# Optimization experiments

Hardware: AMD Instinct MI355X
Metric: run time of the kernel (lower is better)

Reference implementation:

```python
import jax, jax.numpy as jnp
import numpy as np
from jax import lax

B, N, C = 4, 3072, 512
SAMPLE_RATIO = 0.25
CLUSTER_NUM = int(np.ceil(N * SAMPLE_RATIO))  # 768, static (mask=None, no 'r')
K = 5  # self.k, since k <= cluster_num


def setup_inputs() -> dict:
    key = jax.random.key(0)
    k1, = jax.random.split(key, 1)
    x = jax.random.normal(k1, (B, N, C), dtype=jnp.float32)
    # idx_token starts as identity mapping per batch (standard TCFormer init)
    idx_token = jnp.tile(jnp.arange(N, dtype=jnp.int32)[None, :], (B, 1))
    agg_weight = jnp.ones((B, N, 1), dtype=jnp.float32)
    return {"x": x, "idx_token": idx_token, "agg_weight": agg_weight}


def _cluster_dpc_knn(x):
    # runs under no_grad in torch -> stop_gradient here
    xs = lax.stop_gradient(x).astype(jnp.float32)
    sq = jnp.sum(xs * xs, axis=-1)  # [B,N]
    d2 = sq[:, :, None] + sq[:, None, :] - 2.0 * jnp.einsum('bnc,bmc->bnm', xs, xs)
    dist = jnp.sqrt(jnp.maximum(d2, 0.0)) / jnp.sqrt(jnp.float32(C))  # cdist / C**0.5
    # k nearest (smallest) distances
    neg_nearest, _ = lax.top_k(-dist, K)
    dist_nearest = -neg_nearest  # [B,N,K]
    density = jnp.exp(-jnp.mean(dist_nearest ** 2, axis=-1))
    density = density + jax.random.uniform(jax.random.key(42), density.shape, dtype=density.dtype) * 1e-6
    mask = (density[:, None, :] > density[:, :, None]).astype(x.dtype)  # [B,N,N]
    dist_max = jnp.max(dist.reshape(B, -1), axis=-1)[:, None, None]
    dist_min = jnp.min(dist * mask + dist_max * (1.0 - mask), axis=-1)  # [B,N]
    score = dist_min * density
    _, index_down = lax.top_k(score, CLUSTER_NUM)  # [B,cluster]
    # gather rows of dist at cluster centers, assign each token to nearest center
    dmat = jnp.take_along_axis(dist, index_down[:, :, None], axis=1)  # [B,cluster,N]
    idx_cluster = jnp.argmin(dmat, axis=1).astype(jnp.int32)  # [B,N]
    # force centers to map to their own cluster id
    idx_cluster = idx_cluster.at[jnp.arange(B)[:, None], index_down].set(
        jnp.broadcast_to(jnp.arange(CLUSTER_NUM, dtype=jnp.int32)[None, :], (B, CLUSTER_NUM)))
    return idx_cluster


def reference(x, idx_token, agg_weight):
    idx_cluster = _cluster_dpc_knn(x)
    # merge_tokens
    token_weight = jnp.ones((B, N, 1), dtype=x.dtype)
    idx = idx_cluster + jnp.arange(B, dtype=jnp.int32)[:, None] * CLUSTER_NUM  # [B,N]
    idx_flat = idx.reshape(-1)
    all_weight = jax.ops.segment_sum(token_weight.reshape(-1), idx_flat,
                                     num_segments=B * CLUSTER_NUM) + 1e-6  # [B*cluster]
    norm_weight = token_weight / all_weight[idx_flat].reshape(B, N, 1)  # [B,N,1]
    x_merged = jax.ops.segment_sum((x * norm_weight).reshape(B * N, C), idx_flat,
                                   num_segments=B * CLUSTER_NUM).reshape(B, CLUSTER_NUM, C)
    idx_token_new = jnp.take_along_axis(idx_cluster, idx_token, axis=1)  # [B,N]
    weight_t = jnp.take_along_axis(norm_weight, idx_token[:, :, None], axis=1)  # [B,N,1]
    agg_weight_new = agg_weight * weight_t
    return x_merged, agg_weight_new, idx_token_new, idx_cluster
```

## Files before the change

### kernel.cpp

```cpp
#include <hip/hip_runtime.h>
#include <math.h>
#include <float.h>

constexpr int B  = 4;
constexpr int N  = 3072;
constexpr int C  = 512;
constexpr int CL = 768;

typedef unsigned short u16;
typedef __attribute__((ext_vector_type(8))) short s16x8;
typedef __attribute__((ext_vector_type(4))) float f32x4;

__device__ __forceinline__ unsigned rotl32(unsigned v, int d) { return (v << d) | (v >> (32 - d)); }

__device__ inline void threefry2x32(unsigned k0, unsigned k1, unsigned c0, unsigned c1,
                                    unsigned& o0, unsigned& o1) {
  unsigned ks0 = k0, ks1 = k1, ks2 = 0x1BD11BDAu ^ k0 ^ k1;
  unsigned x0 = c0 + ks0, x1 = c1 + ks1;
#define TF_RND(r) { x0 += x1; x1 = rotl32(x1, (r)); x1 ^= x0; }
  TF_RND(13) TF_RND(15) TF_RND(26) TF_RND(6)  x0 += ks1; x1 += ks2 + 1u;
  TF_RND(17) TF_RND(29) TF_RND(16) TF_RND(24) x0 += ks2; x1 += ks0 + 2u;
  TF_RND(13) TF_RND(15) TF_RND(26) TF_RND(6)  x0 += ks0; x1 += ks1 + 3u;
  TF_RND(17) TF_RND(29) TF_RND(16) TF_RND(24) x0 += ks1; x1 += ks2 + 4u;
  TF_RND(13) TF_RND(15) TF_RND(26) TF_RND(6)  x0 += ks2; x1 += ks0 + 5u;
#undef TF_RND
  o0 = x0; o1 = x1;
}

__device__ inline float jax_uniform_bn(int f) {
  constexpr int HALF = (B * N) / 2;
  unsigned o0, o1, bits;
  if (f < HALF) { threefry2x32(0u, 42u, (unsigned)f, (unsigned)(f + HALF), o0, o1); bits = o0; }
  else          { threefry2x32(0u, 42u, (unsigned)(f - HALF), (unsigned)f, o0, o1); bits = o1; }
  return __uint_as_float((bits >> 9) | 0x3f800000u) - 1.0f;
}

__device__ __forceinline__ u16 bf16rn(float f) {
  unsigned u = __float_as_uint(f);
  unsigned r = u + 0x7FFFu + ((u >> 16) & 1u);
  return (u16)(r >> 16);
}
__device__ __forceinline__ float bf16tof(u16 h) {
  return __uint_as_float(((unsigned)h) << 16);
}

__global__ __launch_bounds__(64) void k_prep(const float* __restrict__ x, float* __restrict__ sq,
                                             u16* __restrict__ xhi, u16* __restrict__ xlo,
                                             int* __restrict__ counts,
                                             unsigned long long* __restrict__ packed) {
  int row = blockIdx.x;
  int lane = threadIdx.x;
  const float* xr = x + (size_t)row * C;
  u16* hr = xhi + (size_t)row * C;
  u16* lr = xlo + (size_t)row * C;
  float s = 0.f;
  for (int c = lane * 4; c < C; c += 256) {
    float4 v = *(const float4*)(xr + c);
    s += v.x * v.x + v.y * v.y + v.z * v.z + v.w * v.w;
    u16 h0 = bf16rn(v.x), h1 = bf16rn(v.y), h2 = bf16rn(v.z), h3 = bf16rn(v.w);
    u16 l0 = bf16rn(v.x - bf16tof(h0));
    u16 l1 = bf16rn(v.y - bf16tof(h1));
    u16 l2 = bf16rn(v.z - bf16tof(h2));
    u16 l3 = bf16rn(v.w - bf16tof(h3));
    uint2 hp, lp;
    hp.x = (unsigned)h0 | ((unsigned)h1 << 16); hp.y = (unsigned)h2 | ((unsigned)h3 << 16);
    lp.x = (unsigned)l0 | ((unsigned)l1 << 16); lp.y = (unsigned)l2 | ((unsigned)l3 << 16);
    *(uint2*)(hr + c) = hp;
    *(uint2*)(lr + c) = lp;
  }
  for (int o = 32; o > 0; o >>= 1) s += __shfl_down(s, o, 64);
  if (lane == 0) {
    sq[row] = s;
    packed[row] = ~0ull;
    if (row < B * CL) counts[row] = 0;
  }
}

__device__ __forceinline__ void ins5b(float t[5], float v) {
  float c = v;
  float n;
  n = fminf(t[0], c); c = fmaxf(t[0], c); t[0] = n;
  n = fminf(t[1], c); c = fmaxf(t[1], c); t[1] = n;
  n = fminf(t[2], c); c = fmaxf(t[2], c); t[2] = n;
  n = fminf(t[3], c); c = fmaxf(t[3], c); t[3] = n;
  t[4] = fminf(t[4], c);
}

constexpr int NT3 = N / 128;
constexpr int NTILE3 = NT3 * (NT3 + 1) / 2;

__global__ __launch_bounds__(256, 3) void k_distm(const u16* __restrict__ xhi, const u16* __restrict__ xlo,
                                                  const float* __restrict__ sq,
                                                  float* __restrict__ distbuf,
                                                  float* __restrict__ part5, int b0) {
  constexpr int ASTR = 40;
  __shared__ __align__(16) char smem[40960];
  u16* sAh = (u16*)smem;
  u16* sAl = sAh + 128 * ASTR;
  u16* sBh = sAl + 128 * ASTR;
  u16* sBl = sBh + 128 * ASTR;

  int bl = blockIdx.y, b = b0 + bl;
  int idx = blockIdx.x;
  int ti = 0, rem = idx;
  while (rem >= NT3 - ti) { rem -= NT3 - ti; ++ti; }
  int tj = ti + rem;
  int i0 = ti * 128, j0 = tj * 128;
  bool do_mirror = (ti != tj);

  const float* sqb = sq + (size_t)b * N;
  float* dist = distbuf + (size_t)bl * N * N;

  int tid = threadIdx.x;
  int srow = tid >> 1, shalf = (tid & 1) * 16;
  const u16* gAh = xhi + ((size_t)b * N + i0 + srow) * C + shalf;
  const u16* gAl = xlo + ((size_t)b * N + i0 + srow) * C + shalf;
  const u16* gBh = xhi + ((size_t)b * N + j0 + srow) * C + shalf;
  const u16* gBl = xlo + ((size_t)b * N + j0 + srow) * C + shalf;
  int wofs = srow * ASTR + shalf;

  int lane = tid & 63, w = tid >> 6;
  int wr = (w >> 1) * 64, wc = (w & 1) * 64;
  int l15 = lane & 15, l4 = lane >> 4;

  f32x4 acc[4][4];
#pragma unroll
  for (int rt = 0; rt < 4; ++rt)
#pragma unroll
    for (int ct = 0; ct < 4; ++ct)
#pragma unroll
      for (int e = 0; e < 4; ++e) acc[rt][ct][e] = 0.f;

  uint4 p0 = *(const uint4*)gAh, p1 = *(const uint4*)(gAh + 8);
  uint4 p2 = *(const uint4*)gAl, p3 = *(const uint4*)(gAl + 8);
  uint4 p4 = *(const uint4*)gBh, p5 = *(const uint4*)(gBh + 8);
  uint4 p6 = *(const uint4*)gBl, p7 = *(const uint4*)(gBl + 8);

  for (int k0 = 0; k0 < C; k0 += 32) {
    *(uint4*)&sAh[wofs] = p0; *(uint4*)&sAh[wofs + 8] = p1;
    *(uint4*)&sAl[wofs] = p2; *(uint4*)&sAl[wofs + 8] = p3;
    *(uint4*)&sBh[wofs] = p4; *(uint4*)&sBh[wofs + 8] = p5;
    *(uint4*)&sBl[wofs] = p6; *(uint4*)&sBl[wofs + 8] = p7;
    __syncthreads();
    int kn = k0 + 32;
    if (kn < C) {
      p0 = *(const uint4*)(gAh + kn); p1 = *(const uint4*)(gAh + kn + 8);
      p2 = *(const uint4*)(gAl + kn); p3 = *(const uint4*)(gAl + kn + 8);
      p4 = *(const uint4*)(gBh + kn); p5 = *(const uint4*)(gBh + kn + 8);
      p6 = *(const uint4*)(gBl + kn); p7 = *(const uint4*)(gBl + kn + 8);
    }
    s16x8 ah[4], al[4];
#pragma unroll
    for (int rt = 0; rt < 4; ++rt) {
      int ro = (wr + rt * 16 + l15) * ASTR + l4 * 8;
      ah[rt] = *(const s16x8*)&sAh[ro];
      al[rt] = *(const s16x8*)&sAl[ro];
    }
#pragma unroll
    for (int ct = 0; ct < 4; ++ct) {
      int co = (wc + ct * 16 + l15) * ASTR + l4 * 8;
      s16x8 bh = *(const s16x8*)&sBh[co];
      s16x8 bl = *(const s16x8*)&sBl[co];
#pragma unroll
      for (int rt = 0; rt < 4; ++rt) {
        acc[rt][ct] = __builtin_amdgcn_mfma_f32_16x16x32_bf16(ah[rt], bh, acc[rt][ct], 0, 0, 0);
        acc[rt][ct] = __builtin_amdgcn_mfma_f32_16x16x32_bf16(ah[rt], bl, acc[rt][ct], 0, 0, 0);
        acc[rt][ct] = __builtin_amdgcn_mfma_f32_16x16x32_bf16(al[rt], bh, acc[rt][ct], 0, 0, 0);
      }
    }
    __syncthreads();
  }

  const float SQC = 22.627416997969522f;
  float sqi[4][4], sqj[4];
#pragma unroll
  for (int rt = 0; rt < 4; ++rt)
#pragma unroll
    for (int r = 0; r < 4; ++r) sqi[rt][r] = sqb[i0 + wr + rt * 16 + l4 * 4 + r];
#pragma unroll
  for (int ct = 0; ct < 4; ++ct) sqj[ct] = sqb[j0 + wc + ct * 16 + l15];

#pragma unroll
  for (int rt = 0; rt < 4; ++rt)
#pragma unroll
    for (int ct = 0; ct < 4; ++ct)
#pragma unroll
      for (int r = 0; r < 4; ++r) {
        float d2 = fmaxf(sqi[rt][r] + sqj[ct] - 2.0f * acc[rt][ct][r], 0.0f);
        acc[rt][ct][r] = sqrtf(d2) / SQC;
      }

  constexpr int TSTR = 76;
  float* sT = (float*)smem + w * (32 * TSTR);

  float t5A[5] = {FLT_MAX, FLT_MAX, FLT_MAX, FLT_MAX, FLT_MAX};
  float mxA = 0.f;

#pragma unroll
  for (int p = 0; p < 2; ++p) {
#pragma unroll
    for (int cth = 0; cth < 2; ++cth) {
      int ct = p * 2 + cth;
      int cl = cth * 16 + l15;
#pragma unroll
      for (int rt = 0; rt < 4; ++rt)
#pragma unroll
        for (int r = 0; r < 4; ++r)
          sT[cl * TSTR + rt * 16 + l4 * 4 + r] = acc[rt][ct][r];
    }
    {
      int g4 = lane & 7, rbase = lane >> 3;
#pragma unroll
      for (int it = 0; it < 8; ++it) {
        int rl = it * 8 + rbase;
        float4 v = make_float4(sT[(4 * g4 + 0) * TSTR + rl],
                               sT[(4 * g4 + 1) * TSTR + rl],
                               sT[(4 * g4 + 2) * TSTR + rl],
                               sT[(4 * g4 + 3) * TSTR + rl]);
        *(float4*)(dist + (size_t)(i0 + wr + rl) * N + j0 + wc + p * 32 + 4 * g4) = v;
      }
    }
    if (do_mirror) {
      int cg = lane >> 4, rq = lane & 15;
#pragma unroll
      for (int cc = 0; cc < 8; ++cc) {
        int c = cc * 4 + cg;
        float4 v = *(const float4*)&sT[c * TSTR + rq * 4];
        *(float4*)(dist + (size_t)(j0 + wc + p * 32 + c) * N + i0 + wr + rq * 4) = v;
      }
    }
    for (int c = 0; c < 32; ++c) {
      float v = sT[c * TSTR + lane];
      mxA = fmaxf(mxA, v);
      ins5b(t5A, v);
    }
    if (do_mirror) {
      int cl = lane & 31, half = lane >> 5;
      float t5B[5] = {FLT_MAX, FLT_MAX, FLT_MAX, FLT_MAX, FLT_MAX};
      float mxB = 0.f;
      for (int k = 0; k < 32; ++k) {
        float v = sT[cl * TSTR + half * 32 + k];
        mxB = fmaxf(mxB, v);
        ins5b(t5B, v);
      }
      mxB = fmaxf(mxB, __shfl_xor(mxB, 32, 64));
      float o0 = __shfl_xor(t5B[0], 32, 64);
      float o1 = __shfl_xor(t5B[1], 32, 64);
      float o2 = __shfl_xor(t5B[2], 32, 64);
      float o3 = __shfl_xor(t5B[3], 32, 64);
      float o4 = __shfl_xor(t5B[4], 32, 64);
      ins5b(t5B, o0); ins5b(t5B, o1); ins5b(t5B, o2); ins5b(t5B, o3); ins5b(t5B, o4);
      if (half == 0) {
        int rowB = j0 + wc + p * 32 + cl;
        int slotB = ti * 2 + (wr >> 6);
        float* dst = part5 + (((size_t)bl * 48 + slotB) * 6) * N + rowB;
        dst[0] = t5B[0]; dst[(size_t)N] = t5B[1]; dst[2 * (size_t)N] = t5B[2];
        dst[3 * (size_t)N] = t5B[3]; dst[4 * (size_t)N] = t5B[4]; dst[5 * (size_t)N] = mxB;
      }
    }
  }
  {
    int rowA = i0 + wr + lane;
    int slotA = tj * 2 + (wc >> 6);
    float* dst = part5 + (((size_t)bl * 48 + slotA) * 6) * N + rowA;
    dst[0] = t5A[0]; dst[(size_t)N] = t5A[1]; dst[2 * (size_t)N] = t5A[2];
    dst[3 * (size_t)N] = t5A[3]; dst[4 * (size_t)N] = t5A[4]; dst[5 * (size_t)N] = mxA;
  }
}

__global__ __launch_bounds__(256) void k_dens(const float* __restrict__ part5,
                                              float* __restrict__ density,
                                              float* __restrict__ rowmax, int b0) {
  int g = blockIdx.x * 256 + threadIdx.x;
  int bl = g / N, r = g % N;
  int b = b0 + bl;
  const float* base = part5 + (size_t)bl * 48 * 6 * N + r;
  float t5[5] = {FLT_MAX, FLT_MAX, FLT_MAX, FLT_MAX, FLT_MAX};
  float mx = 0.f;
  for (int s = 0; s < 48; ++s) {
    const float* sp = base + (size_t)s * 6 * N;
    ins5b(t5, sp[0]);
    ins5b(t5, sp[(size_t)N]);
    ins5b(t5, sp[2 * (size_t)N]);
    ins5b(t5, sp[3 * (size_t)N]);
    ins5b(t5, sp[4 * (size_t)N]);
    mx = fmaxf(mx, sp[5 * (size_t)N]);
  }
  float sum = t5[0] * t5[0] + t5[1] * t5[1] + t5[2] * t5[2] + t5[3] * t5[3] + t5[4] * t5[4];
  density[b * N + r] = expf(-(sum / 5.0f)) + jax_uniform_bn(b * N + r) * 1e-6f;
  rowmax[b * N + r] = mx;
}

__global__ __launch_bounds__(1024) void k_dmax(const float* __restrict__ rowmax,
                                               float* __restrict__ distmax) {
  __shared__ float red[16];
  int b = blockIdx.x;
  int tid = threadIdx.x;
  const float* rb = rowmax + (size_t)b * N;
  float mx = 0.f;
  for (int j = tid; j < N; j += 1024) mx = fmaxf(mx, rb[j]);
#pragma unroll
  for (int m = 1; m < 64; m <<= 1) mx = fmaxf(mx, __shfl_xor(mx, m, 64));
  if ((tid & 63) == 0) red[tid >> 6] = mx;
  __syncthreads();
  if (tid == 0) {
    float r = red[0];
#pragma unroll
    for (int q = 1; q < 16; ++q) r = fmaxf(r, red[q]);
    distmax[b] = r;
  }
}

__global__ __launch_bounds__(256) void k_maskmin(const float* __restrict__ distbuf,
                                                 const float* __restrict__ density,
                                                 const float* __restrict__ distmax,
                                                 float* __restrict__ score, int b0) {
  __shared__ float sd[N];
  int tid = threadIdx.x;
  int wv = tid >> 6, lane = tid & 63;
  int i = blockIdx.x * 4 + wv;
  int bl = blockIdx.y, b = b0 + bl;
  const float* db = density + (size_t)b * N;
  for (int j = tid * 4; j < N; j += 1024) *(float4*)(sd + j) = *(const float4*)(db + j);
  __syncthreads();
  float di = sd[i];
  float dmax = distmax[b];
  const float* row = distbuf + ((size_t)bl * N + i) * N;
  float mn = dmax;
#pragma unroll
  for (int it = 0; it < N / 256; ++it) {
    int j = it * 256 + lane * 4;
    float4 v = *(const float4*)(row + j);
    float4 d = *(const float4*)(sd + j);
    mn = fminf(mn, (d.x > di) ? v.x : dmax);
    mn = fminf(mn, (d.y > di) ? v.y : dmax);
    mn = fminf(mn, (d.z > di) ? v.z : dmax);
    mn = fminf(mn, (d.w > di) ? v.w : dmax);
  }
#pragma unroll
  for (int m = 1; m < 64; m <<= 1) mn = fminf(mn, __shfl_xor(mn, m, 64));
  if (lane == 0) score[b * N + i] = mn * di;
}

__global__ __launch_bounds__(256) void k_rank(const float* __restrict__ score,
                                              int* __restrict__ index_down,
                                              int* __restrict__ rank, int b0) {
  __shared__ float ssc[N];
  int tid = threadIdx.x;
  int wv = tid >> 6, lane = tid & 63;
  int i = blockIdx.x * 4 + wv;
  int b = b0 + blockIdx.y;
  const float* sb = score + (size_t)b * N;
  for (int j = tid * 4; j < N; j += 1024) *(float4*)(ssc + j) = *(const float4*)(sb + j);
  __syncthreads();
  float si = ssc[i];
  int cnt = 0;
#pragma unroll
  for (int it = 0; it < N / 256; ++it) {
    int j = it * 256 + lane * 4;
    float4 v = *(const float4*)(ssc + j);
    cnt += (v.x > si) || (v.x == si && (j + 0) < i);
    cnt += (v.y > si) || (v.y == si && (j + 1) < i);
    cnt += (v.z > si) || (v.z == si && (j + 2) < i);
    cnt += (v.w > si) || (v.w == si && (j + 3) < i);
  }
#pragma unroll
  for (int m = 1; m < 64; m <<= 1) cnt += __shfl_xor(cnt, m, 64);
  if (lane == 0) {
    rank[b * N + i] = (cnt < CL) ? cnt : -1;
    if (cnt < CL) index_down[b * CL + cnt] = i;
  }
}

__global__ __launch_bounds__(256) void k_assign_part(const float* __restrict__ distbuf,
                                                     const int* __restrict__ index_down,
                                                     unsigned long long* __restrict__ packed, int b0) {
  constexpr int RCH = CL / 8;
  __shared__ int sid[RCH];
  int bl = blockIdx.z, b = b0 + bl;
  int r0 = blockIdx.y * RCH;
  int tid = threadIdx.x;
  for (int r = tid; r < RCH; r += 256) sid[r] = index_down[b * CL + r0 + r];
  __syncthreads();
  int j = blockIdx.x * 256 + tid;
  const float* base = distbuf + (size_t)bl * N * N;
  float best = FLT_MAX; int bestr = 0;
#pragma unroll 8
  for (int r = 0; r < RCH; ++r) {
    float d = base[(size_t)sid[r] * N + j];
    if (d < best) { best = d; bestr = r0 + r; }
  }
  unsigned long long key = ((unsigned long long)__float_as_uint(best) << 32) | (unsigned)bestr;
  atomicMin(&packed[b * N + j], key);
}

__global__ void k_assign_fin2(const unsigned long long* __restrict__ packed,
                              const int* __restrict__ rank,
                              int* __restrict__ idx_cluster, int* __restrict__ counts) {
  int g = blockIdx.x * 256 + threadIdx.x;
  int b = g / N;
  int r = rank[g];
  int cl = (r >= 0) ? r : (int)(unsigned)(packed[g] & 0xffffffffull);
  idx_cluster[g] = cl;
  atomicAdd(&counts[b * CL + cl], 1);
}

__global__ __launch_bounds__(1024) void k_scan(const int* __restrict__ counts,
                                               int* __restrict__ offsets, int* __restrict__ cursor) {
  constexpr int T = B * CL;
  __shared__ int sm[T];
  int tid = threadIdx.x;
  for (int p = tid; p < T; p += 1024) sm[p] = counts[p];
  __syncthreads();
  for (int off = 1; off < T; off <<= 1) {
    int v[3]; int n = 0;
    for (int p = tid; p < T; p += 1024) { v[n++] = (p >= off) ? sm[p - off] : 0; }
    __syncthreads();
    n = 0;
    for (int p = tid; p < T; p += 1024) { sm[p] += v[n++]; }
    __syncthreads();
  }
  for (int p = tid; p < T; p += 1024) {
    int e = sm[p] - counts[p];
    offsets[p] = e; cursor[p] = e;
  }
}

__global__ void k_fill(const int* __restrict__ idx_cluster, int* __restrict__ cursor,
                       int* __restrict__ members) {
  int g = blockIdx.x * 256 + threadIdx.x;
  int b = g / N, i = g % N;
  int seg = b * CL + idx_cluster[g];
  int pos = atomicAdd(&cursor[seg], 1);
  members[pos] = i;
}

__global__ __launch_bounds__(128) void k_gather(const float* __restrict__ x, const int* __restrict__ members,
                                                const int* __restrict__ offsets, const int* __restrict__ counts,
                                                float* __restrict__ out0) {
  int seg = blockIdx.x;
  int b = seg / CL;
  int cnt = counts[seg], off = offsets[seg];
  float nw = 1.0f / ((float)cnt + 1e-6f);
  int c = threadIdx.x * 4;
  const float* xb = x + (size_t)b * N * C;
  float4 acc = make_float4(0.f, 0.f, 0.f, 0.f);
  for (int m = 0; m < cnt; ++m) {
    int tok = members[off + m];
    float4 v = *(const float4*)(xb + (size_t)tok * C + c);
    acc.x += v.x * nw; acc.y += v.y * nw; acc.z += v.z * nw; acc.w += v.w * nw;
  }
  *(float4*)(out0 + (size_t)seg * C + c) = acc;
}

__global__ void k_final(const float* __restrict__ agg_weight, const int* __restrict__ idx_token,
                        const int* __restrict__ idx_cluster, const int* __restrict__ counts,
                        float* __restrict__ out1, float* __restrict__ out2, float* __restrict__ out3) {
  int g = blockIdx.x * 256 + threadIdx.x;
  int b = g / N;
  int it = idx_token[g];
  int clt = idx_cluster[b * N + it];
  float nwt = 1.0f / ((float)counts[b * CL + clt] + 1e-6f);
  out1[g] = agg_weight[g] * nwt;
  out2[g] = (float)clt;
  out3[g] = (float)idx_cluster[g];
}

extern "C" void kernel_launch(void* const* d_in, const int* in_sizes, int n_in,
                              void* d_out, int out_size, void* d_ws, size_t ws_size,
                              hipStream_t stream) {
  const float* x          = (const float*)d_in[0];
  const int*   idx_token  = (const int*)d_in[1];
  const float* agg_weight = (const float*)d_in[2];

  float* out0 = (float*)d_out;
  float* out1 = out0 + (size_t)B * CL * C;
  float* out2 = out1 + (size_t)B * N;
  float* out3 = out2 + (size_t)B * N;

  char* w = (char*)d_ws;
  auto carve = [&](size_t bytes) { char* p = w; w += (bytes + 255) & ~(size_t)255; return p; };
  float*    sq         = (float*)carve((size_t)B * N * 4);
  float*    density    = (float*)carve((size_t)B * N * 4);
  float*    score      = (float*)carve((size_t)B * N * 4);
  float*    rowmax     = (float*)carve((size_t)B * N * 4);
  float*    distmax    = (float*)carve((size_t)B * 4);
  int*      index_down = (int*)carve((size_t)B * CL * 4);
  int*      rank       = (int*)carve((size_t)B * N * 4);
  int*      idx_clus   = (int*)carve((size_t)B * N * 4);
  int*      counts     = (int*)carve((size_t)B * CL * 4);
  int*      offsets    = (int*)carve((size_t)B * CL * 4);
  int*      cursor     = (int*)carve((size_t)B * CL * 4);
  int*      members    = (int*)carve((size_t)B * N * 4);
  unsigned long long* packed = (unsigned long long*)carve((size_t)B * N * 8);
  u16*      xhi        = (u16*)carve((size_t)B * N * C * 2);
  u16*      xlo        = (u16*)carve((size_t)B * N * C * 2);
  float*    part5      = (float*)carve((size_t)B * 48 * 6 * N * 4);
  size_t used = (size_t)(w - (char*)d_ws);
  size_t per  = (size_t)N * N * 4;
  int nb_max = (ws_size > used) ? (int)((ws_size - used) / per) : 0;
  if (nb_max < 1) nb_max = 1;
  if (nb_max > B) nb_max = B;
  float* distbuf = (float*)w;

  k_prep<<<B * N, 64, 0, stream>>>(x, sq, xhi, xlo, counts, packed);

  for (int b0 = 0; b0 < B; b0 += nb_max) {
    int nb = (B - b0 < nb_max) ? (B - b0) : nb_max;
    k_distm<<<dim3(NTILE3, nb), 256, 0, stream>>>(xhi, xlo, sq, distbuf, part5, b0);
    k_dens<<<(nb * N) / 256, 256, 0, stream>>>(part5, density, rowmax, b0);
    k_dmax<<<nb, 1024, 0, stream>>>(rowmax + (size_t)b0 * N, distmax + b0);
    k_maskmin<<<dim3(N / 4, nb), 256, 0, stream>>>(distbuf, density, distmax, score, b0);
    k_rank<<<dim3(N / 4, nb), 256, 0, stream>>>(score, index_down, rank, b0);
    k_assign_part<<<dim3(N / 256, 8, nb), 256, 0, stream>>>(distbuf, index_down, packed, b0);
  }

  k_assign_fin2<<<(B * N) / 256, 256, 0, stream>>>(packed, rank, idx_clus, counts);
  k_scan<<<1, 1024, 0, stream>>>(counts, offsets, cursor);
  k_fill<<<(B * N) / 256, 256, 0, stream>>>(idx_clus, cursor, members);
  k_gather<<<B * CL, 128, 0, stream>>>(x, members, offsets, counts, out0);
  k_final<<<(B * N) / 256, 256, 0, stream>>>(agg_weight, idx_token, idx_clus, counts, out1, out2, out3);
}
```

Baseline: 301.7 us.

## Fuse post-distance stages into one cooperative persistent kernel with grid syncs

Replaces the chain of tail kernels (density, dmax, masked min, rank, assign, scan, fill, gather, final) with a single cooperative kernel of 256 blocks that separates the stages with grid.sync(). It also drops the batch chunking loop, so the distance matrix for all batches is computed in one launch. The aim is to remove per-kernel launch and drain gaps between the many small stages. The cost is that each stage now runs on a fixed 256-block grid, which can reduce parallelism in heavy stages such as the masked min (each wave now handles 12 rows) and the assign step (only 384 work units). It also assumes the workspace is large enough to hold all B distance matrices.

```diff
diff --git a/kernel.cpp b/kernel.cpp
--- a/kernel.cpp
+++ b/kernel.cpp
@@ -1,6 +1,9 @@
 #include <hip/hip_runtime.h>
+#include <hip/hip_cooperative_groups.h>
 #include <math.h>
 #include <float.h>
+
+namespace cg = cooperative_groups;
 
 constexpr int B  = 4;
 constexpr int N  = 3072;
@@ -268,202 +271,214 @@
   }
 }
 
-__global__ __launch_bounds__(256) void k_dens(const float* __restrict__ part5,
-                                              float* __restrict__ density,
-                                              float* __restrict__ rowmax, int b0) {
-  int g = blockIdx.x * 256 + threadIdx.x;
-  int bl = g / N, r = g % N;
-  int b = b0 + bl;
-  const float* base = part5 + (size_t)bl * 48 * 6 * N + r;
-  float t5[5] = {FLT_MAX, FLT_MAX, FLT_MAX, FLT_MAX, FLT_MAX};
-  float mx = 0.f;
-  for (int s = 0; s < 48; ++s) {
-    const float* sp = base + (size_t)s * 6 * N;
-    ins5b(t5, sp[0]);
-    ins5b(t5, sp[(size_t)N]);
-    ins5b(t5, sp[2 * (size_t)N]);
-    ins5b(t5, sp[3 * (size_t)N]);
-    ins5b(t5, sp[4 * (size_t)N]);
-    mx = fmaxf(mx, sp[5 * (size_t)N]);
-  }
-  float sum = t5[0] * t5[0] + t5[1] * t5[1] + t5[2] * t5[2] + t5[3] * t5[3] + t5[4] * t5[4];
-  density[b * N + r] = expf(-(sum / 5.0f)) + jax_uniform_bn(b * N + r) * 1e-6f;
-  rowmax[b * N + r] = mx;
-}
-
-__global__ __launch_bounds__(1024) void k_dmax(const float* __restrict__ rowmax,
-                                               float* __restrict__ distmax) {
-  __shared__ float red[16];
-  int b = blockIdx.x;
-  int tid = threadIdx.x;
-  const float* rb = rowmax + (size_t)b * N;
-  float mx = 0.f;
-  for (int j = tid; j < N; j += 1024) mx = fmaxf(mx, rb[j]);
-#pragma unroll
-  for (int m = 1; m < 64; m <<= 1) mx = fmaxf(mx, __shfl_xor(mx, m, 64));
-  if ((tid & 63) == 0) red[tid >> 6] = mx;
-  __syncthreads();
-  if (tid == 0) {
-    float r = red[0];
-#pragma unroll
-    for (int q = 1; q < 16; ++q) r = fmaxf(r, red[q]);
-    distmax[b] = r;
-  }
-}
-
-__global__ __launch_bounds__(256) void k_maskmin(const float* __restrict__ distbuf,
-                                                 const float* __restrict__ density,
-                                                 const float* __restrict__ distmax,
-                                                 float* __restrict__ score, int b0) {
-  __shared__ float sd[N];
+struct TailArgs {
+  const float* part5;
+  float* density;
+  float* rowmax;
+  float* distmax;
+  const float* distbuf;
+  float* score;
+  int* index_down;
+  int* rank;
+  unsigned long long* packed;
+  int* idx_cluster;
+  int* counts;
+  int* offsets;
+  int* cursor;
+  int* members;
+  const float* x;
+  const int* idx_token;
+  const float* agg_weight;
+  float* out0;
+  float* out1;
+  float* out2;
+  float* out3;
+};
+
+constexpr int TGRID = 256;
+
+__global__ __launch_bounds__(256) void k_tail(TailArgs a) {
+  cg::grid_group grid = cg::this_grid();
+  __shared__ float smf[N];
+  __shared__ float sred[16];
   int tid = threadIdx.x;
   int wv = tid >> 6, lane = tid & 63;
-  int i = blockIdx.x * 4 + wv;
-  int bl = blockIdx.y, b = b0 + bl;
-  const float* db = density + (size_t)b * N;
-  for (int j = tid * 4; j < N; j += 1024) *(float4*)(sd + j) = *(const float4*)(db + j);
-  __syncthreads();
-  float di = sd[i];
-  float dmax = distmax[b];
-  const float* row = distbuf + ((size_t)bl * N + i) * N;
-  float mn = dmax;
-#pragma unroll
-  for (int it = 0; it < N / 256; ++it) {
-    int j = it * 256 + lane * 4;
-    float4 v = *(const float4*)(row + j);
-    float4 d = *(const float4*)(sd + j);
-    mn = fminf(mn, (d.x > di) ? v.x : dmax);
-    mn = fminf(mn, (d.y > di) ? v.y : dmax);
-    mn = fminf(mn, (d.z > di) ? v.z : dmax);
-    mn = fminf(mn, (d.w > di) ? v.w : dmax);
-  }
-#pragma unroll
-  for (int m = 1; m < 64; m <<= 1) mn = fminf(mn, __shfl_xor(mn, m, 64));
-  if (lane == 0) score[b * N + i] = mn * di;
-}
-
-__global__ __launch_bounds__(256) void k_rank(const float* __restrict__ score,
-                                              int* __restrict__ index_down,
-                                              int* __restrict__ rank, int b0) {
-  __shared__ float ssc[N];
-  int tid = threadIdx.x;
-  int wv = tid >> 6, lane = tid & 63;
-  int i = blockIdx.x * 4 + wv;
-  int b = b0 + blockIdx.y;
-  const float* sb = score + (size_t)b * N;
-  for (int j = tid * 4; j < N; j += 1024) *(float4*)(ssc + j) = *(const float4*)(sb + j);
-  __syncthreads();
-  float si = ssc[i];
-  int cnt = 0;
-#pragma unroll
-  for (int it = 0; it < N / 256; ++it) {
-    int j = it * 256 + lane * 4;
-    float4 v = *(const float4*)(ssc + j);
-    cnt += (v.x > si) || (v.x == si && (j + 0) < i);
-    cnt += (v.y > si) || (v.y == si && (j + 1) < i);
-    cnt += (v.z > si) || (v.z == si && (j + 2) < i);
-    cnt += (v.w > si) || (v.w == si && (j + 3) < i);
-  }
-#pragma unroll
-  for (int m = 1; m < 64; m <<= 1) cnt += __shfl_xor(cnt, m, 64);
-  if (lane == 0) {
-    rank[b * N + i] = (cnt < CL) ? cnt : -1;
-    if (cnt < CL) index_down[b * CL + cnt] = i;
-  }
-}
-
-__global__ __launch_bounds__(256) void k_assign_part(const float* __restrict__ distbuf,
-                                                     const int* __restrict__ index_down,
-                                                     unsigned long long* __restrict__ packed, int b0) {
-  constexpr int RCH = CL / 8;
-  __shared__ int sid[RCH];
-  int bl = blockIdx.z, b = b0 + bl;
-  int r0 = blockIdx.y * RCH;
-  int tid = threadIdx.x;
-  for (int r = tid; r < RCH; r += 256) sid[r] = index_down[b * CL + r0 + r];
-  __syncthreads();
-  int j = blockIdx.x * 256 + tid;
-  const float* base = distbuf + (size_t)bl * N * N;
-  float best = FLT_MAX; int bestr = 0;
+  int gtid = blockIdx.x * 256 + tid;
+
+  for (int g = gtid; g < B * N; g += TGRID * 256) {
+    int b = g / N, r = g % N;
+    const float* base = a.part5 + (size_t)b * 48 * 6 * N + r;
+    float t5[5] = {FLT_MAX, FLT_MAX, FLT_MAX, FLT_MAX, FLT_MAX};
+    float mx = 0.f;
+    for (int s = 0; s < 48; ++s) {
+      const float* sp = base + (size_t)s * 6 * N;
+      ins5b(t5, sp[0]);
+      ins5b(t5, sp[(size_t)N]);
+      ins5b(t5, sp[2 * (size_t)N]);
+      ins5b(t5, sp[3 * (size_t)N]);
+      ins5b(t5, sp[4 * (size_t)N]);
+      mx = fmaxf(mx, sp[5 * (size_t)N]);
+    }
+    float sum = t5[0] * t5[0] + t5[1] * t5[1] + t5[2] * t5[2] + t5[3] * t5[3] + t5[4] * t5[4];
+    a.density[g] = expf(-(sum / 5.0f)) + jax_uniform_bn(g) * 1e-6f;
+    a.rowmax[g] = mx;
+  }
+  grid.sync();
+
+  if (blockIdx.x < B) {
+    int b = blockIdx.x;
+    float mx = 0.f;
+    for (int j = tid; j < N; j += 256) mx = fmaxf(mx, a.rowmax[b * N + j]);
+#pragma unroll
+    for (int m = 1; m < 64; m <<= 1) mx = fmaxf(mx, __shfl_xor(mx, m, 64));
+    if (lane == 0) sred[wv] = mx;
+    __syncthreads();
+    if (tid == 0)
+      a.distmax[b] = fmaxf(fmaxf(sred[0], sred[1]), fmaxf(sred[2], sred[3]));
+  }
+  grid.sync();
+
+  {
+    int b = blockIdx.x >> 6;
+    int blk = blockIdx.x & 63;
+    const float* db = a.density + (size_t)b * N;
+    for (int j = tid * 4; j < N; j += 1024) *(float4*)(smf + j) = *(const float4*)(db + j);
+    __syncthreads();
+    float dmax = a.distmax[b];
+    for (int t = 0; t < 12; ++t) {
+      int r = blk * 48 + wv * 12 + t;
+      float di = smf[r];
+      const float* row = a.distbuf + (size_t)b * N * N + (size_t)r * N;
+      float mn = dmax;
+#pragma unroll
+      for (int it = 0; it < N / 256; ++it) {
+        int j = it * 256 + lane * 4;
+        float4 v = *(const float4*)(row + j);
+        float4 d = *(const float4*)(smf + j);
+        mn = fminf(mn, (d.x > di) ? v.x : dmax);
+        mn = fminf(mn, (d.y > di) ? v.y : dmax);
+        mn = fminf(mn, (d.z > di) ? v.z : dmax);
+        mn = fminf(mn, (d.w > di) ? v.w : dmax);
+      }
+#pragma unroll
+      for (int m = 1; m < 64; m <<= 1) mn = fminf(mn, __shfl_xor(mn, m, 64));
+      if (lane == 0) a.score[b * N + r] = mn * di;
+    }
+  }
+  grid.sync();
+
+  {
+    int b = blockIdx.x >> 6;
+    int blk = blockIdx.x & 63;
+    const float* sb = a.score + (size_t)b * N;
+    for (int j = tid * 4; j < N; j += 1024) *(float4*)(smf + j) = *(const float4*)(sb + j);
+    __syncthreads();
+    for (int t = 0; t < 12; ++t) {
+      int i = blk * 48 + wv * 12 + t;
+      float si = smf[i];
+      int cnt = 0;
+#pragma unroll
+      for (int it = 0; it < N / 256; ++it) {
+        int j = it * 256 + lane * 4;
+        float4 v = *(const float4*)(smf + j);
+        cnt += (v.x > si) || (v.x == si && (j + 0) < i);
+        cnt += (v.y > si) || (v.y == si && (j + 1) < i);
+        cnt += (v.z > si) || (v.z == si && (j + 2) < i);
+        cnt += (v.w > si) || (v.w == si && (j + 3) < i);
+      }
+#pragma unroll
+      for (int m = 1; m < 64; m <<= 1) cnt += __shfl_xor(cnt, m, 64);
+      if (lane == 0) {
+        a.rank[b * N + i] = (cnt < CL) ? cnt : -1;
+        if (cnt < CL) a.index_down[b * CL + cnt] = i;
+      }
+    }
+  }
+  grid.sync();
+
+  {
+    int* ssid = (int*)smf;
+    for (int u = blockIdx.x; u < 384; u += TGRID) {
+      int b = u / 96, rem2 = u % 96, rch = rem2 / 12, jb = rem2 % 12;
+      __syncthreads();
+      if (tid < 96) ssid[tid] = a.index_down[b * CL + rch * 96 + tid];
+      __syncthreads();
+      int j = jb * 256 + tid;
+      const float* base = a.distbuf + (size_t)b * N * N;
+      float best = FLT_MAX; int bestr = 0;
 #pragma unroll 8
-  for (int r = 0; r < RCH; ++r) {
-    float d = base[(size_t)sid[r] * N + j];
-    if (d < best) { best = d; bestr = r0 + r; }
-  }
-  unsigned long long key = ((unsigned long long)__float_as_uint(best) << 32) | (unsigned)bestr;
-  atomicMin(&packed[b * N + j], key);
-}
-
-__global__ void k_assign_fin2(const unsigned long long* __restrict__ packed,
-                              const int* __restrict__ rank,
-                              int* __restrict__ idx_cluster, int* __restrict__ counts) {
-  int g = blockIdx.x * 256 + threadIdx.x;
-  int b = g / N;
-  int r = rank[g];
-  int cl = (r >= 0) ? r : (int)(unsigned)(packed[g] & 0xffffffffull);
-  idx_cluster[g] = cl;
-  atomicAdd(&counts[b * CL + cl], 1);
-}
-
-__global__ __launch_bounds__(1024) void k_scan(const int* __restrict__ counts,
-                                               int* __restrict__ offsets, int* __restrict__ cursor) {
-  constexpr int T = B * CL;
-  __shared__ int sm[T];
-  int tid = threadIdx.x;
-  for (int p = tid; p < T; p += 1024) sm[p] = counts[p];
-  __syncthreads();
-  for (int off = 1; off < T; off <<= 1) {
-    int v[3]; int n = 0;
-    for (int p = tid; p < T; p += 1024) { v[n++] = (p >= off) ? sm[p - off] : 0; }
+      for (int r = 0; r < 96; ++r) {
+        float d = base[(size_t)ssid[r] * N + j];
+        if (d < best) { best = d; bestr = rch * 96 + r; }
+      }
+      unsigned long long key = ((unsigned long long)__float_as_uint(best) << 32) | (unsigned)bestr;
+      atomicMin(&a.packed[(size_t)b * N + j], key);
+    }
+  }
+  grid.sync();
+
+  for (int g = gtid; g < B * N; g += TGRID * 256) {
+    int b = g / N;
+    int r = a.rank[g];
+    int cl = (r >= 0) ? r : (int)(unsigned)(a.packed[g] & 0xffffffffull);
+    a.idx_cluster[g] = cl;
+    atomicAdd(&a.counts[b * CL + cl], 1);
+  }
+  grid.sync();
+
+  if (blockIdx.x == 0) {
+    int* sm = (int*)smf;
+    constexpr int T = B * CL;
+    for (int p = tid; p < T; p += 256) sm[p] = a.counts[p];
     __syncthreads();
-    n = 0;
-    for (int p = tid; p < T; p += 1024) { sm[p] += v[n++]; }
-    __syncthreads();
-  }
-  for (int p = tid; p < T; p += 1024) {
-    int e = sm[p] - counts[p];
-    offsets[p] = e; cursor[p] = e;
-  }
-}
-
-__global__ void k_fill(const int* __restrict__ idx_cluster, int* __restrict__ cursor,
-                       int* __restrict__ members) {
-  int g = blockIdx.x * 256 + threadIdx.x;
-  int b = g / N, i = g % N;
-  int seg = b * CL + idx_cluster[g];
-  int pos = atomicAdd(&cursor[seg], 1);
-  members[pos] = i;
-}
-
-__global__ __launch_bounds__(128) void k_gather(const float* __restrict__ x, const int* __restrict__ members,
-                                                const int* __restrict__ offsets, const int* __restrict__ counts,
-                                                float* __restrict__ out0) {
-  int seg = blockIdx.x;
-  int b = seg / CL;
-  int cnt = counts[seg], off = offsets[seg];
-  float nw = 1.0f / ((float)cnt + 1e-6f);
-  int c = threadIdx.x * 4;
-  const float* xb = x + (size_t)b * N * C;
-  float4 acc = make_float4(0.f, 0.f, 0.f, 0.f);
-  for (int m = 0; m < cnt; ++m) {
-    int tok = members[off + m];
-    float4 v = *(const float4*)(xb + (size_t)tok * C + c);
-    acc.x += v.x * nw; acc.y += v.y * nw; acc.z += v.z * nw; acc.w += v.w * nw;
-  }
-  *(float4*)(out0 + (size_t)seg * C + c) = acc;
-}
-
-__global__ void k_final(const float* __restrict__ agg_weight, const int* __restrict__ idx_token,
-                        const int* __restrict__ idx_cluster, const int* __restrict__ counts,
-                        float* __restrict__ out1, float* __restrict__ out2, float* __restrict__ out3) {
-  int g = blockIdx.x * 256 + threadIdx.x;
-  int b = g / N;
-  int it = idx_token[g];
-  int clt = idx_cluster[b * N + it];
-  float nwt = 1.0f / ((float)counts[b * CL + clt] + 1e-6f);
-  out1[g] = agg_weight[g] * nwt;
-  out2[g] = (float)clt;
-  out3[g] = (float)idx_cluster[g];
+    for (int off = 1; off < T; off <<= 1) {
+      int v[12]; int n = 0;
+      for (int p = tid; p < T; p += 256) { v[n++] = (p >= off) ? sm[p - off] : 0; }
+      __syncthreads();
+      n = 0;
+      for (int p = tid; p < T; p += 256) { sm[p] += v[n++]; }
+      __syncthreads();
+    }
+    for (int p = tid; p < T; p += 256) {
+      int e = sm[p] - a.counts[p];
+      a.offsets[p] = e; a.cursor[p] = e;
+    }
+  }
+  grid.sync();
+
+  for (int g = gtid; g < B * N; g += TGRID * 256) {
+    int b = g / N, i = g % N;
+    int seg = b * CL + a.idx_cluster[g];
+    int pos = atomicAdd(&a.cursor[seg], 1);
+    a.members[pos] = i;
+  }
+  grid.sync();
+
+  for (int it = 0; it < 6; ++it) {
+    int seg = blockIdx.x * 2 + (tid >> 7) + it * 512;
+    int b = seg / CL;
+    int cnt = a.counts[seg], off = a.offsets[seg];
+    float nw = 1.0f / ((float)cnt + 1e-6f);
+    int c = (tid & 127) * 4;
+    const float* xb = a.x + (size_t)b * N * C;
+    float4 accv = make_float4(0.f, 0.f, 0.f, 0.f);
+    for (int m = 0; m < cnt; ++m) {
+      int tok = a.members[off + m];
+      float4 v = *(const float4*)(xb + (size_t)tok * C + c);
+      accv.x += v.x * nw; accv.y += v.y * nw; accv.z += v.z * nw; accv.w += v.w * nw;
+    }
+    *(float4*)(a.out0 + (size_t)seg * C + c) = accv;
+  }
+
+  for (int g = gtid; g < B * N; g += TGRID * 256) {
+    int b = g / N;
+    int it = a.idx_token[g];
+    int clt = a.idx_cluster[b * N + it];
+    float nwt = 1.0f / ((float)a.counts[b * CL + clt] + 1e-6f);
+    a.out1[g] = a.agg_weight[g] * nwt;
+    a.out2[g] = (float)clt;
+    a.out3[g] = (float)a.idx_cluster[g];
+  }
 }
 
 extern "C" void kernel_launch(void* const* d_in, const int* in_sizes, int n_in,
@@ -496,28 +511,17 @@
   u16*      xhi        = (u16*)carve((size_t)B * N * C * 2);
   u16*      xlo        = (u16*)carve((size_t)B * N * C * 2);
   float*    part5      = (float*)carve((size_t)B * 48 * 6 * N * 4);
-  size_t used = (size_t)(w - (char*)d_ws);
-  size_t per  = (size_t)N * N * 4;
-  int nb_max = (ws_size > used) ? (int)((ws_size - used) / per) : 0;
-  if (nb_max < 1) nb_max = 1;
-  if (nb_max > B) nb_max = B;
-  float* distbuf = (float*)w;
+  float*    distbuf    = (float*)w;
 
   k_prep<<<B * N, 64, 0, stream>>>(x, sq, xhi, xlo, counts, packed);
-
-  for (int b0 = 0; b0 < B; b0 += nb_max) {
-    int nb = (B - b0 < nb_max) ? (B - b0) : nb_max;
-    k_distm<<<dim3(NTILE3, nb), 256, 0, stream>>>(xhi, xlo, sq, distbuf, part5, b0);
-    k_dens<<<(nb * N) / 256, 256, 0, stream>>>(part5, density, rowmax, b0);
-    k_dmax<<<nb, 1024, 0, stream>>>(rowmax + (size_t)b0 * N, distmax + b0);
-    k_maskmin<<<dim3(N / 4, nb), 256, 0, stream>>>(distbuf, density, distmax, score, b0);
-    k_rank<<<dim3(N / 4, nb), 256, 0, stream>>>(score, index_down, rank, b0);
-    k_assign_part<<<dim3(N / 256, 8, nb), 256, 0, stream>>>(distbuf, index_down, packed, b0);
-  }
-
-  k_assign_fin2<<<(B * N) / 256, 256, 0, stream>>>(packed, rank, idx_clus, counts);
-  k_scan<<<1, 1024, 0, stream>>>(counts, offsets, cursor);
-  k_fill<<<(B * N) / 256, 256, 0, stream>>>(idx_clus, cursor, members);
-  k_gather<<<B * CL, 128, 0, stream>>>(x, members, offsets, counts, out0);
-  k_final<<<(B * N) / 256, 256, 0, stream>>>(agg_weight, idx_token, idx_clus, counts, out1, out2, out3);
-}
+  k_distm<<<dim3(NTILE3, B), 256, 0, stream>>>(xhi, xlo, sq, distbuf, part5, 0);
+
+  TailArgs ta;
+  ta.part5 = part5; ta.density = density; ta.rowmax = rowmax; ta.distmax = distmax;
+  ta.distbuf = distbuf; ta.score = score; ta.index_down = index_down; ta.rank = rank;
+  ta.packed = packed; ta.idx_cluster = idx_clus; ta.counts = counts; ta.offsets = offsets;
+  ta.cursor = cursor; ta.members = members; ta.x = x; ta.idx_token = idx_token;
+  ta.agg_weight = agg_weight; ta.out0 = out0; ta.out1 = out1; ta.out2 = out2; ta.out3 = out3;
+  void* kargs[] = { (void*)&ta };
+  hipLaunchCooperativeKernel((const void*)k_tail, dim3(TGRID), dim3(256), kargs, 0, stream);
+}
```

New measurement: 587.8 us. 1.95x slower.
